# Kernel optimization log

Measured on AMD Instinct MI355X. Metric: run time of the kernel, lower is better.

## Reference

```python
import jax, jax.numpy as jnp
import numpy as np

N_NODES = 20000   # num_of_nodes + 1 (incl. prediction node)
FEAT = 256        # in_features == hidden_features == out_features
N_LAYERS = 2
ALPHA = 0.2       # LeakyReLU negative slope
V_OBS = 512       # observed codes per patient
D_H = np.sqrt(FEAT * 1.0)  # sqrt(hidden_features * num_of_heads), n_heads=1
EPS = 1e-6


def _fc_edges(nodes):
    # torch: source = nodes.repeat(1, n); dest = each node repeated n times
    n = len(nodes)
    return np.stack([np.tile(nodes, n), np.repeat(nodes, n)]).astype(np.int64)


def setup_inputs() -> dict:
    key = jax.random.key(0)
    ks = jax.random.split(key, 16)
    rng = np.random.default_rng(0)
    obs = np.sort(rng.choice(np.arange(1, N_NODES - 1), size=V_OBS, replace=False))
    input_edges = jnp.asarray(_fc_edges(obs))
    obs_out = np.concatenate([obs, [N_NODES - 1]])  # add prediction node
    output_edges = jnp.asarray(_fc_edges(obs_out))

    s = 0.02
    embed = s * jax.random.normal(ks[0], (N_NODES, FEAT), jnp.float32)
    embed = embed.at[0].set(0.0)  # padding_idx=0
    return {
        "embed": embed,
        "W_w": s * jax.random.normal(ks[1], (N_LAYERS, FEAT, FEAT), jnp.float32),
        "W_b": s * jax.random.normal(ks[2], (N_LAYERS, FEAT), jnp.float32),
        "a": s * jax.random.normal(ks[3], (N_LAYERS, 2 * FEAT), jnp.float32),
        "ln_a": jnp.ones((N_LAYERS, FEAT), jnp.float32),
        "ln_b": jnp.zeros((N_LAYERS, FEAT), jnp.float32),
        "Wo_w": s * jax.random.normal(ks[4], (FEAT, FEAT), jnp.float32),
        "Wo_b": s * jax.random.normal(ks[5], (FEAT,), jnp.float32),
        "ao": s * jax.random.normal(ks[6], (2 * FEAT,), jnp.float32),
        "lno_a": jnp.ones((FEAT,), jnp.float32),
        "lno_b": jnp.zeros((FEAT,), jnp.float32),
        "lin_w": s * jax.random.normal(ks[7], (FEAT, FEAT), jnp.float32),
        "lin_b": s * jax.random.normal(ks[8], (FEAT,), jnp.float32),
        "param_w": s * jax.random.normal(ks[9], (2 * FEAT, FEAT), jnp.float32),
        "param_b": s * jax.random.normal(ks[10], (2 * FEAT,), jnp.float32),
        "out1_w": s * jax.random.normal(ks[11], (FEAT, FEAT), jnp.float32),
        "out1_b": s * jax.random.normal(ks[12], (FEAT,), jnp.float32),
        "out2_w": s * jax.random.normal(ks[13], (1, FEAT), jnp.float32),
        "out2_b": s * jax.random.normal(ks[14], (1,), jnp.float32),
        "input_edges": input_edges,
        "output_edges": output_edges,
    }


def _attention(x, edges, Ww, Wb, avec):
    # d = Linear(x): (N, H)
    d = x @ Ww.T + Wb
    H = d.shape[1]
    # a . [d_src ; d_dst] == (d @ a_left)[src] + (d @ a_right)[dst]  (cheaper, same math)
    s_node = d @ avec[:H]
    t_node = d @ avec[H:]
    score = s_node[edges[0]] + t_node[edges[1]]                  # (E,)
    e = jnp.exp(jax.nn.leaky_relu(score, ALPHA) / D_H)           # unnormalized attn
    n = x.shape[0]
    rowsum = jax.ops.segment_sum(e, edges[0], num_segments=n)   # (N,)
    agg = jax.ops.segment_sum(e[:, None] * d[edges[1]], edges[0], num_segments=n)
    zero = rowsum == 0
    # rows with no in-edges get an identity self-edge of weight 1 and rowsum 1
    agg = agg + jnp.where(zero[:, None], d, 0.0)
    return agg / jnp.where(zero, 1.0, rowsum)[:, None]


def _layernorm(x, g, b):
    m = x.mean(-1, keepdims=True)
    s = jnp.std(x, axis=-1, ddof=1, keepdims=True)  # torch std: unbiased
    return g * (x - m) / (s + EPS) + b


def reference(embed, W_w, W_b, a, ln_a, ln_b, Wo_w, Wo_b, ao, lno_a, lno_b,
              lin_w, lin_b, param_w, param_b, out1_w, out1_b, out2_w, out2_b,
              input_edges, output_edges):
    h = embed  # embedding lookup of arange(N) == the full table
    for l in range(N_LAYERS):  # in_att stack, concat=True, n_heads=1: ffn = LN -> ELU
        h = jax.nn.elu(_layernorm(_attention(h, input_edges, W_w[l], W_b[l], a[l]),
                                  ln_a[l], ln_b[l]))
    # variational layer (eval mode: reparameterize returns mu)
    hp = (h @ param_w.T + param_b).reshape(-1, 2, FEAT)
    h = hp[:, 0, :]  # mu
    # out_att: concat=False, mean over 1 head; ffn = LN -> ReLU -> Linear
    g = _attention(h, output_edges, Wo_w, Wo_b, ao)
    g = jax.nn.relu(_layernorm(g, lno_a, lno_b)) @ lin_w.T + lin_b
    # out_layer on prediction node: ReLU -> Linear -> ReLU -> Linear(->1)
    z = jax.nn.relu(g[-1])
    z = jax.nn.relu(z @ out1_w.T + out1_b)
    logit = z @ out2_w.T + out2_b  # (1,)
    return logit
```

## Files before the change

kernel.cpp:

```cpp
#include <hip/hip_runtime.h>
#include <hip/hip_bf16.h>

#define FEAT 256
#define NOBS 512
#define NOUT 513
#define GAT_ALPHA 0.2f
#define INV_DH (1.0f / 16.0f)
#define LN_EPS 1e-6f


__device__ __forceinline__ float b2f(unsigned short u) {
    union { float f; unsigned v; } x;
    x.v = ((unsigned)u) << 16;
    return x.f;
}

__device__ __forceinline__ float loadv(const void* p, long idx, int isbf) {
    if (isbf) return b2f(((const unsigned short*)p)[idx]);
    return ((const float*)p)[idx];
}

__device__ __forceinline__ float4 load4(const void* p, long idx, int isbf) {
    if (isbf) {
        ushort4 u = *(const ushort4*)((const unsigned short*)p + idx);
        return make_float4(b2f(u.x), b2f(u.y), b2f(u.z), b2f(u.w));
    }
    return *(const float4*)((const float*)p + idx);
}

__device__ __forceinline__ int detect_bf(const void* w) {
    const unsigned short* hb = (const unsigned short*)w;
    int sane = 0;
#pragma unroll
    for (int i = 0; i < 32; i += 2) {
        float a = fabsf(b2f(hb[i]));
        sane += (a > 1e-4f && a < 0.3f) ? 1 : 0;
    }
    return (sane >= 8) ? 1 : 0;
}

__device__ __forceinline__ int detect_estep(const void* edges) {
    const int* ei = (const int*)edges;
    return (ei[1] == 0 && ei[3] == 0 && ei[5] == 0 && ei[7] == 0) ? 2 : 1;
}

__device__ __forceinline__ float wave_allreduce(float v) {
#pragma unroll
    for (int o = 1; o < 64; o <<= 1) v += __shfl_xor(v, o);
    return v;
}

__device__ __forceinline__ float bsum1024(float v, float* red) {
    __syncthreads();
    float s = wave_allreduce(v);
    int lane = threadIdx.x & 63, w = threadIdx.x >> 6;
    if (lane == 0) red[w] = s;
    __syncthreads();
    float t = 0.f;
#pragma unroll
    for (int i = 0; i < 16; i++) t += red[i];
    return t;
}

#define FV_AS0 0
#define FV_AS1 256
#define FV_AT0 512
#define FV_AT1 768
#define FV_WB0 1024
#define FV_WB1 1280
#define FV_LNA0 1536
#define FV_LNA1 1792
#define FV_LNB0 2048
#define FV_LNB1 2304
#define FV_WOB 2560
#define FV_AOS 2816
#define FV_AOT 3072
#define FV_LNOA 3328
#define FV_LNOB 3584
#define FV_LINB 3840
#define FV_PARB 4096
#define FV_O1B 4352
#define FV_O2W 4608
#define FV_O2B 4864

__global__ __launch_bounds__(256) void k_front(
        const void* embed, const void* W_w, const void* W_b, const void* a,
        const void* ln_a, const void* ln_b, const void* Wo_w, const void* Wo_b,
        const void* ao, const void* lno_a, const void* lno_b, const void* lin_w,
        const void* lin_b, const void* param_w, const void* param_b,
        const void* out1_w, const void* out1_b, const void* out2_w, const void* out2_b,
        const void* oedges, float* fv, float* packs,
        float* __restrict__ D1, float* S1, float* T1, int* done) {
    __shared__ __align__(16) char smem[37888];
    float (*xs)[FEAT] = (float(*)[FEAT])smem;
    float (*wl)[33] = (float(*)[33])(smem + 4096);
    float (*tile)[65] = (float(*)[65])smem;
    int isbf = detect_bf(W_w);
    int b = blockIdx.x, tid = threadIdx.x, lane = tid & 63, w = tid >> 6;
    if (b < 129) {
        int estep = detect_estep(oedges);
        int i0 = b << 2;
        int nr = NOUT - i0;
        if (nr > 4) nr = 4;
        if (w < nr) {
            const int* oe = (const int*)oedges;
            long node = oe[(long)(i0 + w) * estep];
            *(float4*)&xs[w][lane << 2] = load4(embed, node * FEAT + (lane << 2), isbf);
        } else {
#pragma unroll
            for (int q = 0; q < 4; q++) xs[w][(lane << 2) + q] = 0.f;
        }
        float acc[4] = {0.f, 0.f, 0.f, 0.f};
        int fb8 = tid >> 3;
        int kq = tid & 7;
        for (int kc = 0; kc < 8; kc++) {
            int k0 = kc << 5;
            __syncthreads();
#pragma unroll
            for (int i = 0; i < 8; i++) {
                int f = fb8 + (i << 5);
                float4 v = load4(W_w, (long)f * FEAT + k0 + (kq << 2), isbf);
                wl[f][(kq << 2) + 0] = v.x;
                wl[f][(kq << 2) + 1] = v.y;
                wl[f][(kq << 2) + 2] = v.z;
                wl[f][(kq << 2) + 3] = v.w;
            }
            __syncthreads();
#pragma unroll
            for (int k4 = 0; k4 < 8; k4++) {
                float4 x0 = ((const float4*)xs[0])[(kc << 3) + k4];
                float4 x1 = ((const float4*)xs[1])[(kc << 3) + k4];
                float4 x2 = ((const float4*)xs[2])[(kc << 3) + k4];
                float4 x3 = ((const float4*)xs[3])[(kc << 3) + k4];
                float xa0[4] = {x0.x, x0.y, x0.z, x0.w};
                float xa1[4] = {x1.x, x1.y, x1.z, x1.w};
                float xa2[4] = {x2.x, x2.y, x2.z, x2.w};
                float xa3[4] = {x3.x, x3.y, x3.z, x3.w};
#pragma unroll
                for (int j = 0; j < 4; j++) {
                    float wv = wl[tid][(k4 << 2) + j];
                    acc[0] += xa0[j] * wv;
                    acc[1] += xa1[j] * wv;
                    acc[2] += xa2[j] * wv;
                    acc[3] += xa3[j] * wv;
                }
            }
        }
        float bb = loadv(W_b, tid, isbf);
#pragma unroll
        for (int j = 0; j < 4; j++) acc[j] += bb;
#pragma unroll
        for (int j = 0; j < 4; j++)
            if (j < nr) D1[(long)(i0 + j) * FEAT + tid] = acc[j];
        __syncthreads();
#pragma unroll
        for (int j = 0; j < 4; j++) xs[j][tid] = acc[j];
        __syncthreads();
        if (w < nr) {
            float sv = 0.f, tv = 0.f;
#pragma unroll
            for (int q = 0; q < 4; q++) {
                int f = lane + (q << 6);
                float dv = xs[w][f];
                sv += dv * loadv(a, f, isbf);
                tv += dv * loadv(a, FEAT + f, isbf);
            }
            sv = wave_allreduce(sv);
            tv = wave_allreduce(tv);
            if (lane == 0) { S1[i0 + w] = sv; T1[i0 + w] = tv; }
        }
    } else if (b < 209) {
        int job = b - 129;
        int m = 1 + (job >> 4), t = job & 15;
        int f0 = (t >> 2) << 6, k0 = (t & 3) << 6;
        const void* base;
        long eoff = 0;
        switch (m) {
            case 1: base = W_w; eoff = 65536; break;
            case 2: base = param_w; break;
            case 3: base = Wo_w; break;
            case 4: base = lin_w; break;
            default: base = out1_w; break;
        }
        int r = tid >> 2, cq = (tid & 3) << 4;
#pragma unroll
        for (int jj = 0; jj < 4; jj++) {
            float4 v = load4(base, eoff + (long)(f0 + r) * FEAT + k0 + cq + (jj << 2), isbf);
            tile[r][cq + (jj << 2) + 0] = v.x;
            tile[r][cq + (jj << 2) + 1] = v.y;
            tile[r][cq + (jj << 2) + 2] = v.z;
            tile[r][cq + (jj << 2) + 3] = v.w;
        }
        __syncthreads();
        float4* pack = (float4*)(packs + (long)m * 65536);
#pragma unroll
        for (int it = 0; it < 4; it++) {
            int kk = ((w << 2) + it) << 2;
            float4 v = make_float4(tile[lane][kk], tile[lane][kk + 1],
                                   tile[lane][kk + 2], tile[lane][kk + 3]);
            int k4g = (k0 >> 2) + (w << 2) + it;
            pack[(k4g << 8) + f0 + lane] = v;
        }
    } else {
        int cid = b - 209;
        const void* s;
        long so = 0;
        float* d;
        int n = 256;
        switch (cid) {
            case 0:  s = a;       so = 0;   d = fv + FV_AS0;  break;
            case 1:  s = a;       so = 512; d = fv + FV_AS1;  break;
            case 2:  s = a;       so = 256; d = fv + FV_AT0;  break;
            case 3:  s = a;       so = 768; d = fv + FV_AT1;  break;
            case 4:  s = W_b;     so = 0;   d = fv + FV_WB0;  break;
            case 5:  s = W_b;     so = 256; d = fv + FV_WB1;  break;
            case 6:  s = ln_a;    so = 0;   d = fv + FV_LNA0; break;
            case 7:  s = ln_a;    so = 256; d = fv + FV_LNA1; break;
            case 8:  s = ln_b;    so = 0;   d = fv + FV_LNB0; break;
            case 9:  s = ln_b;    so = 256; d = fv + FV_LNB1; break;
            case 10: s = Wo_b;    so = 0;   d = fv + FV_WOB;  break;
            case 11: s = ao;      so = 0;   d = fv + FV_AOS;  break;
            case 12: s = ao;      so = 256; d = fv + FV_AOT;  break;
            case 13: s = lno_a;   so = 0;   d = fv + FV_LNOA; break;
            case 14: s = lno_b;   so = 0;   d = fv + FV_LNOB; break;
            case 15: s = lin_b;   so = 0;   d = fv + FV_LINB; break;
            case 16: s = param_b; so = 0;   d = fv + FV_PARB; break;
            case 17: s = out1_b;  so = 0;   d = fv + FV_O1B;  break;
            case 18: s = out2_w;  so = 0;   d = fv + FV_O2W;  break;
            default: s = out2_b;  so = 0;   d = fv + FV_O2B;  n = 1; break;
        }
        for (int idx = tid; idx < n; idx += FEAT) d[idx] = loadv(s, so + idx, isbf);
        if (cid == 19 && tid == 0)
            __hip_atomic_store(done, 0, __ATOMIC_RELAXED, __HIP_MEMORY_SCOPE_AGENT);
    }
}

__device__ void tail_head(const float* __restrict__ D, const float* __restrict__ S,
                          const float* __restrict__ T, const float* __restrict__ fv,
                          const float4* __restrict__ PL, const float4* __restrict__ PO1,
                          int isbf, void* out, float* e, float (*wacc)[FEAT],
                          float (*part)[FEAT], float* ys, float* zs, float* red) {
    int tid = threadIdx.x, lane = tid & 63, w = tid >> 6;
    float sN = S[NOUT - 1];
    float p = 0.f;
    if (tid < NOUT) {
        float sc = sN + T[tid];
        sc = (sc > 0.f ? sc : GAT_ALPHA * sc) * INV_DH;
        float ev = __expf(sc);
        e[tid] = ev;
        p = ev;
    }
    float rowsum = bsum1024(p, red);
    float4 a4 = make_float4(0.f, 0.f, 0.f, 0.f);
    for (int j = w; j < NOUT; j += 16) {
        float ej = e[j];
        float4 dv = *(const float4*)(D + (long)j * FEAT + (lane << 2));
        a4.x += ej * dv.x; a4.y += ej * dv.y;
        a4.z += ej * dv.z; a4.w += ej * dv.w;
    }
    *(float4*)&wacc[w][lane << 2] = a4;
    __syncthreads();
    float val = 0.f;
    if (tid < FEAT) {
#pragma unroll
        for (int q = 0; q < 16; q++) val += wacc[q][tid];
        val /= rowsum;
    }
    float m = bsum1024(tid < FEAT ? val : 0.f, red) * (1.f / FEAT);
    float dv = (tid < FEAT) ? val - m : 0.f;
    float var = bsum1024(dv * dv, red) * (1.f / (FEAT - 1));
    if (tid < FEAT) {
        float y = fv[FV_LNOA + tid] * dv / (sqrtf(var) + LN_EPS) + fv[FV_LNOB + tid];
        ys[tid] = fmaxf(y, 0.f);
    }
    __syncthreads();
    int f = tid & 255, kq = tid >> 8;
    float g = 0.f;
#pragma unroll
    for (int q = 0; q < 16; q++) {
        int k4 = (kq << 4) + q;
        float4 wv = PL[(k4 << 8) + f];
        float4 yv = ((const float4*)ys)[k4];
        g += yv.x * wv.x + yv.y * wv.y + yv.z * wv.z + yv.w * wv.w;
    }
    part[kq][f] = g;
    __syncthreads();
    if (tid < FEAT) {
        float gg = part[0][tid] + part[1][tid] + part[2][tid] + part[3][tid] + fv[FV_LINB + tid];
        zs[tid] = fmaxf(gg, 0.f);
    }
    __syncthreads();
    float g2 = 0.f;
#pragma unroll
    for (int q = 0; q < 16; q++) {
        int k4 = (kq << 4) + q;
        float4 wv = PO1[(k4 << 8) + f];
        float4 zv = ((const float4*)zs)[k4];
        g2 += zv.x * wv.x + zv.y * wv.y + zv.z * wv.z + zv.w * wv.w;
    }
    __syncthreads();
    part[kq][f] = g2;
    __syncthreads();
    float z2 = 0.f;
    if (tid < FEAT) {
        z2 = part[0][tid] + part[1][tid] + part[2][tid] + part[3][tid] + fv[FV_O1B + tid];
        z2 = fmaxf(z2, 0.f);
        z2 *= fv[FV_O2W + tid];
    }
    float logit = bsum1024(z2, red) + fv[FV_O2B];
    if (tid == 0) {
        if (isbf) ((__hip_bfloat16*)out)[0] = __float2bfloat16(logit);
        else ((float*)out)[0] = logit;
    }
}

template <bool PWO, bool TAIL>
__global__ __launch_bounds__(1024) void k_mid(
        const float* __restrict__ Din, const float* __restrict__ Sin,
        const float* __restrict__ Tin, const float* __restrict__ ga,
        const float* __restrict__ gb, const float4* __restrict__ W1,
        const float* __restrict__ b1, const float4* __restrict__ W2,
        const float* __restrict__ b2v, const float* __restrict__ as_,
        const float* __restrict__ at_, float* __restrict__ Dout,
        float* Sout, float* Tout,
        const float* fvFull, const float4* PL, const float4* PO1,
        const void* dtypeP, int* done, void* out) {
    __shared__ __align__(16) float e[2][NOBS];
    __shared__ __align__(16) float sacc[16][2][FEAT];
    __shared__ __align__(16) float xs[2][FEAT];
    __shared__ __align__(16) float part[4][2][FEAT];
    __shared__ float redA[16];
    __shared__ float redB[16];
    __shared__ float rsh[2];
    __shared__ int lastflag;
    int tid = threadIdx.x, lane = tid & 63, w = tid >> 6;
    int b = blockIdx.x;
    bool fb = (b == 256);
    int i0 = b << 1;
    int nr = fb ? 1 : 2;
    int row = (tid >> 8) & 1, f = tid & 255;

    float val = 0.f;
    if (!fb) {
        int rr = tid >> 9, j = tid & 511;
        float sc = Sin[i0 + rr] + Tin[j];
        sc = (sc > 0.f ? sc : GAT_ALPHA * sc) * INV_DH;
        e[rr][j] = __expf(sc);
        __syncthreads();
        int r2 = w >> 3, seg = w & 7;
        float pv = wave_allreduce(e[r2][(seg << 6) + lane]);
        if (lane == 0) redA[w] = pv;
        __syncthreads();
        if (tid < 2) {
            float s = 0.f;
#pragma unroll
            for (int q = 0; q < 8; q++) s += redA[(tid << 3) + q];
            rsh[tid] = s;
        }
        float4 a0 = make_float4(0.f, 0.f, 0.f, 0.f), a1 = a0;
        for (int j2 = w; j2 < NOBS; j2 += 16) {
            float4 dv = *(const float4*)(Din + (long)j2 * FEAT + (lane << 2));
            float e0 = e[0][j2], e1 = e[1][j2];
            a0.x += e0 * dv.x; a0.y += e0 * dv.y; a0.z += e0 * dv.z; a0.w += e0 * dv.w;
            a1.x += e1 * dv.x; a1.y += e1 * dv.y; a1.z += e1 * dv.z; a1.w += e1 * dv.w;
        }
        *(float4*)&sacc[w][0][lane << 2] = a0;
        *(float4*)&sacc[w][1][lane << 2] = a1;
        __syncthreads();
        if (tid < 512) {
#pragma unroll
            for (int q = 0; q < 16; q++) val += sacc[q][row][f];
            val /= rsh[row];
        }
    } else {
        if (tid < 512) val = (row == 0) ? Din[(long)NOBS * FEAT + f] : 0.f;
    }

    __syncthreads();
    float s1 = wave_allreduce(tid < 512 ? val : 0.f);
    if (lane == 0) redA[w] = s1;
    __syncthreads();
    float m = (redA[(row << 2)] + redA[(row << 2) + 1] +
               redA[(row << 2) + 2] + redA[(row << 2) + 3]) * (1.f / FEAT);
    float dvv = (tid < 512) ? val - m : 0.f;
    __syncthreads();
    float s2 = wave_allreduce(dvv * dvv);
    if (lane == 0) redA[w] = s2;
    __syncthreads();
    float var = (redA[(row << 2)] + redA[(row << 2) + 1] +
                 redA[(row << 2) + 2] + redA[(row << 2) + 3]) * (1.f / (FEAT - 1));
    if (tid < 512) {
        float isd = 1.f / (sqrtf(var) + LN_EPS);
        float y = ga[f] * dvv * isd + gb[f];
        xs[row][f] = (y > 0.f) ? y : (__expf(y) - 1.f);
    }
    __syncthreads();

    int q = tid >> 8;
    float ac0 = 0.f, ac1 = 0.f;
#pragma unroll
    for (int t = 0; t < 16; t++) {
        int k4 = (q << 4) + t;
        float4 wv = W1[(k4 << 8) + f];
        float4 x0 = ((const float4*)xs[0])[k4];
        float4 x1 = ((const float4*)xs[1])[k4];
        ac0 += x0.x * wv.x + x0.y * wv.y + x0.z * wv.z + x0.w * wv.w;
        ac1 += x1.x * wv.x + x1.y * wv.y + x1.z * wv.z + x1.w * wv.w;
    }
    part[q][0][f] = ac0;
    part[q][1][f] = ac1;
    __syncthreads();
    float dval = 0.f;
    if (tid < 512)
        dval = part[0][row][f] + part[1][row][f] + part[2][row][f] + part[3][row][f] + b1[f];
    if (PWO) {
        __syncthreads();
        if (tid < 512) xs[row][f] = dval;
        __syncthreads();
        float bc0 = 0.f, bc1 = 0.f;
#pragma unroll
        for (int t = 0; t < 16; t++) {
            int k4 = (q << 4) + t;
            float4 wv = W2[(k4 << 8) + f];
            float4 x0 = ((const float4*)xs[0])[k4];
            float4 x1 = ((const float4*)xs[1])[k4];
            bc0 += x0.x * wv.x + x0.y * wv.y + x0.z * wv.z + x0.w * wv.w;
            bc1 += x1.x * wv.x + x1.y * wv.y + x1.z * wv.z + x1.w * wv.w;
        }
        __syncthreads();
        part[q][0][f] = bc0;
        part[q][1][f] = bc1;
        __syncthreads();
        if (tid < 512)
            dval = part[0][row][f] + part[1][row][f] + part[2][row][f] + part[3][row][f] + b2v[f];
    }
    if (tid < 512 && row < nr)
        Dout[(long)(i0 + row) * FEAT + f] = dval;

    __syncthreads();
    float sv = wave_allreduce(tid < 512 ? dval * as_[f] : 0.f);
    float tv = wave_allreduce(tid < 512 ? dval * at_[f] : 0.f);
    if (lane == 0) { redA[w] = sv; redB[w] = tv; }
    __syncthreads();
    if (tid < nr) {
        float ss = redA[(tid << 2)] + redA[(tid << 2) + 1] +
                   redA[(tid << 2) + 2] + redA[(tid << 2) + 3];
        float tt = redB[(tid << 2)] + redB[(tid << 2) + 1] +
                   redB[(tid << 2) + 2] + redB[(tid << 2) + 3];
        Sout[i0 + tid] = ss;
        Tout[i0 + tid] = tt;
    }

    if (TAIL) {
        __syncthreads();
        if (tid == 0) {
            __threadfence();
            int old = atomicAdd(done, 1);
            lastflag = (old == 256) ? 1 : 0;
        }
        __syncthreads();
        if (lastflag) {
            if (tid == 0) __threadfence();
            __syncthreads();
            int isbf = detect_bf(dtypeP);
            tail_head(Dout, Sout, Tout, fvFull, PL, PO1, isbf, out,
                      (float*)e, (float(*)[FEAT])sacc, (float(*)[FEAT])part,
                      (float*)part + 4 * FEAT, (float*)part + 5 * FEAT, redA);
        }
    }
}

extern "C" void kernel_launch(void* const* d_in, const int* in_sizes, int n_in,
                              void* d_out, int out_size, void* d_ws, size_t ws_size,
                              hipStream_t stream) {
    const void* embed = d_in[0];
    const void* W_w = d_in[1];
    const void* W_b = d_in[2];
    const void* a = d_in[3];
    const void* ln_a = d_in[4];
    const void* ln_b = d_in[5];
    const void* Wo_w = d_in[6];
    const void* Wo_b = d_in[7];
    const void* ao = d_in[8];
    const void* lno_a = d_in[9];
    const void* lno_b = d_in[10];
    const void* lin_w = d_in[11];
    const void* lin_b = d_in[12];
    const void* param_w = d_in[13];
    const void* param_b = d_in[14];
    const void* out1_w = d_in[15];
    const void* out1_b = d_in[16];
    const void* out2_w = d_in[17];
    const void* out2_b = d_in[18];
    const void* oedges = d_in[20];

    char* ws = (char*)d_ws;
    int* done = (int*)ws;
    float* fv = (float*)(ws + 256);
    float* packs = (float*)(ws + 32768);
    float* D1 = (float*)(ws + 1605632);
    float* D2 = (float*)(ws + 2131200);
    float* S1 = (float*)(ws + 2656768);
    float* T1 = (float*)(ws + 2660864);
    float* S2 = (float*)(ws + 2664960);
    float* T2 = (float*)(ws + 2669056);

    const float4* P1 = (const float4*)(packs + 1 * 65536);
    const float4* PP = (const float4*)(packs + 2 * 65536);
    const float4* PWo = (const float4*)(packs + 3 * 65536);
    const float4* PL = (const float4*)(packs + 4 * 65536);
    const float4* PO1 = (const float4*)(packs + 5 * 65536);

    k_front<<<229, FEAT, 0, stream>>>(embed, W_w, W_b, a, ln_a, ln_b, Wo_w, Wo_b, ao,
                                      lno_a, lno_b, lin_w, lin_b, param_w, param_b,
                                      out1_w, out1_b, out2_w, out2_b, oedges,
                                      fv, packs, D1, S1, T1, done);
    k_mid<false, false><<<257, 1024, 0, stream>>>(D1, S1, T1, fv + FV_LNA0, fv + FV_LNB0,
                                                  P1, fv + FV_WB1, nullptr, nullptr,
                                                  fv + FV_AS1, fv + FV_AT1, D2, S2, T2,
                                                  nullptr, nullptr, nullptr, nullptr,
                                                  nullptr, nullptr);
    k_mid<true, true><<<257, 1024, 0, stream>>>(D2, S2, T2, fv + FV_LNA1, fv + FV_LNB1,
                                                PP, fv + FV_PARB, PWo, fv + FV_WOB,
                                                fv + FV_AOS, fv + FV_AOT, D1, S1, T1,
                                                fv, PL, PO1, W_w, done, d_out);
}
```

Baseline: 96.88 us.

## Fuse three kernels into one persistent kernel with software grid barriers

Replaces the front kernel and the two mid kernels with a single 256-block persistent kernel. The stages are separated by atomic-counter grid barriers, and a memset resets the counters before launch. The prediction node's row is now computed by the last-finishing block through a serial chain of matrix-vector products instead of as an extra block in each stage, and stores use nontemporal hints. This aims to remove kernel launch gaps and the odd 257th block, at the cost of spin-wait barriers that depend on all 256 blocks being co-resident and on a serial tail.

```diff
diff --git a/kernel.cpp b/kernel.cpp
--- a/kernel.cpp
+++ b/kernel.cpp
@@ -4,9 +4,12 @@
 #define FEAT 256
 #define NOBS 512
 #define NOUT 513
+#define NBLK 256
 #define GAT_ALPHA 0.2f
 #define INV_DH (1.0f / 16.0f)
 #define LN_EPS 1e-6f
+
+typedef float f32x4 __attribute__((ext_vector_type(4)));
 
 
 __device__ __forceinline__ float b2f(unsigned short u) {
@@ -60,6 +63,24 @@
 #pragma unroll
     for (int i = 0; i < 16; i++) t += red[i];
     return t;
+}
+
+__device__ __forceinline__ void ntst(float* p, float v) { __builtin_nontemporal_store(v, p); }
+__device__ __forceinline__ void ntst4(float* p, float4 v) {
+    f32x4 t = {v.x, v.y, v.z, v.w};
+    __builtin_nontemporal_store(t, (f32x4*)p);
+}
+
+__device__ __forceinline__ void gsync(int* bar, int idx) {
+    __syncthreads();
+    if (threadIdx.x == 0) {
+        __threadfence();
+        atomicAdd(&bar[idx], 1);
+        while (__hip_atomic_load(&bar[idx], __ATOMIC_RELAXED, __HIP_MEMORY_SCOPE_AGENT) < NBLK)
+            __builtin_amdgcn_s_sleep(2);
+        __threadfence();
+    }
+    __syncthreads();
 }
 
 #define FV_AS0 0
@@ -83,126 +104,297 @@
 #define FV_O2W 4608
 #define FV_O2B 4864
 
-__global__ __launch_bounds__(256) void k_front(
+#define O_E 0
+#define O_SACC 4096
+#define O_XS 36864
+#define O_PART 38912
+#define O_REDA 47104
+#define O_REDB 47168
+#define O_RSH 47232
+#define O_FLAG 47240
+#define SMEM_BYTES 47360
+
+__device__ __forceinline__ void mv1024(const float4* __restrict__ P, const float* __restrict__ bias,
+                                       const float* __restrict__ xin, float* __restrict__ dst,
+                                       float (*part)[FEAT]) {
+    int tid = threadIdx.x, f = tid & 255, kq = tid >> 8;
+    float g = 0.f;
+#pragma unroll
+    for (int t = 0; t < 16; t++) {
+        int k4 = (kq << 4) + t;
+        float4 wv = P[(k4 << 8) + f];
+        float4 xv = ((const float4*)xin)[k4];
+        g += xv.x * wv.x + xv.y * wv.y + xv.z * wv.z + xv.w * wv.w;
+    }
+    __syncthreads();
+    part[kq][f] = g;
+    __syncthreads();
+    if (tid < FEAT) dst[tid] = part[0][tid] + part[1][tid] + part[2][tid] + part[3][tid] + bias[tid];
+    __syncthreads();
+}
+
+__device__ __forceinline__ void ln_elu(float* v, const float* ga, const float* gb, float* red) {
+    int tid = threadIdx.x;
+    float x = (tid < FEAT) ? v[tid] : 0.f;
+    float m = bsum1024(x, red) * (1.f / FEAT);
+    float d = (tid < FEAT) ? x - m : 0.f;
+    float var = bsum1024(d * d, red) * (1.f / (FEAT - 1));
+    if (tid < FEAT) {
+        float y = ga[tid] * d / (sqrtf(var) + LN_EPS) + gb[tid];
+        v[tid] = (y > 0.f) ? y : (__expf(y) - 1.f);
+    }
+    __syncthreads();
+}
+
+template <bool PWO>
+__device__ __forceinline__ void stage_mid(char* smem,
+        const float* __restrict__ Din, const float* __restrict__ Sin,
+        const float* __restrict__ Tin, const float* __restrict__ ga,
+        const float* __restrict__ gb, const float4* __restrict__ W1,
+        const float* __restrict__ b1, const float4* __restrict__ W2,
+        const float* __restrict__ b2v, const float* __restrict__ as_,
+        const float* __restrict__ at_, float* __restrict__ Dout,
+        float* Sout, float* Tout) {
+    float (*e)[NOBS] = (float(*)[NOBS])(smem + O_E);
+    float (*sacc)[2][FEAT] = (float(*)[2][FEAT])(smem + O_SACC);
+    float (*xs)[FEAT] = (float(*)[FEAT])(smem + O_XS);
+    float (*part)[2][FEAT] = (float(*)[2][FEAT])(smem + O_PART);
+    float* redA = (float*)(smem + O_REDA);
+    float* redB = (float*)(smem + O_REDB);
+    float* rsh = (float*)(smem + O_RSH);
+    int tid = threadIdx.x, lane = tid & 63, w = tid >> 6;
+    int b = blockIdx.x;
+    int i0 = b << 1;
+    int row = (tid >> 8) & 1, f = tid & 255;
+
+    int rr = tid >> 9, j = tid & 511;
+    float sc = Sin[i0 + rr] + Tin[j];
+    sc = (sc > 0.f ? sc : GAT_ALPHA * sc) * INV_DH;
+    e[rr][j] = __expf(sc);
+    __syncthreads();
+    int r2 = w >> 3, seg = w & 7;
+    float pv = wave_allreduce(e[r2][(seg << 6) + lane]);
+    if (lane == 0) redA[w] = pv;
+    __syncthreads();
+    if (tid < 2) {
+        float s = 0.f;
+#pragma unroll
+        for (int q = 0; q < 8; q++) s += redA[(tid << 3) + q];
+        rsh[tid] = s;
+    }
+    float4 a0 = make_float4(0.f, 0.f, 0.f, 0.f), a1 = a0;
+    for (int j2 = w; j2 < NOBS; j2 += 16) {
+        float4 dv = *(const float4*)(Din + (long)j2 * FEAT + (lane << 2));
+        float e0 = e[0][j2], e1 = e[1][j2];
+        a0.x += e0 * dv.x; a0.y += e0 * dv.y; a0.z += e0 * dv.z; a0.w += e0 * dv.w;
+        a1.x += e1 * dv.x; a1.y += e1 * dv.y; a1.z += e1 * dv.z; a1.w += e1 * dv.w;
+    }
+    *(float4*)&sacc[w][0][lane << 2] = a0;
+    *(float4*)&sacc[w][1][lane << 2] = a1;
+    __syncthreads();
+    float val = 0.f;
+    if (tid < 512) {
+#pragma unroll
+        for (int q = 0; q < 16; q++) val += sacc[q][row][f];
+        val /= rsh[row];
+    }
+    __syncthreads();
+    float s1 = wave_allreduce(tid < 512 ? val : 0.f);
+    if (lane == 0) redA[w] = s1;
+    __syncthreads();
+    float m = (redA[(row << 2)] + redA[(row << 2) + 1] +
+               redA[(row << 2) + 2] + redA[(row << 2) + 3]) * (1.f / FEAT);
+    float dvv = (tid < 512) ? val - m : 0.f;
+    __syncthreads();
+    float s2 = wave_allreduce(dvv * dvv);
+    if (lane == 0) redA[w] = s2;
+    __syncthreads();
+    float var = (redA[(row << 2)] + redA[(row << 2) + 1] +
+                 redA[(row << 2) + 2] + redA[(row << 2) + 3]) * (1.f / (FEAT - 1));
+    if (tid < 512) {
+        float isd = 1.f / (sqrtf(var) + LN_EPS);
+        float y = ga[f] * dvv * isd + gb[f];
+        xs[row][f] = (y > 0.f) ? y : (__expf(y) - 1.f);
+    }
+    __syncthreads();
+    int q = tid >> 8;
+    float ac0 = 0.f, ac1 = 0.f;
+#pragma unroll
+    for (int t = 0; t < 16; t++) {
+        int k4 = (q << 4) + t;
+        float4 wv = W1[(k4 << 8) + f];
+        float4 x0 = ((const float4*)xs[0])[k4];
+        float4 x1 = ((const float4*)xs[1])[k4];
+        ac0 += x0.x * wv.x + x0.y * wv.y + x0.z * wv.z + x0.w * wv.w;
+        ac1 += x1.x * wv.x + x1.y * wv.y + x1.z * wv.z + x1.w * wv.w;
+    }
+    part[q][0][f] = ac0;
+    part[q][1][f] = ac1;
+    __syncthreads();
+    float dval = 0.f;
+    if (tid < 512)
+        dval = part[0][row][f] + part[1][row][f] + part[2][row][f] + part[3][row][f] + b1[f];
+    if (PWO) {
+        __syncthreads();
+        if (tid < 512) xs[row][f] = dval;
+        __syncthreads();
+        float bc0 = 0.f, bc1 = 0.f;
+#pragma unroll
+        for (int t = 0; t < 16; t++) {
+            int k4 = (q << 4) + t;
+            float4 wv = W2[(k4 << 8) + f];
+            float4 x0 = ((const float4*)xs[0])[k4];
+            float4 x1 = ((const float4*)xs[1])[k4];
+            bc0 += x0.x * wv.x + x0.y * wv.y + x0.z * wv.z + x0.w * wv.w;
+            bc1 += x1.x * wv.x + x1.y * wv.y + x1.z * wv.z + x1.w * wv.w;
+        }
+        __syncthreads();
+        part[q][0][f] = bc0;
+        part[q][1][f] = bc1;
+        __syncthreads();
+        if (tid < 512)
+            dval = part[0][row][f] + part[1][row][f] + part[2][row][f] + part[3][row][f] + b2v[f];
+    }
+    if (tid < 512) ntst(&Dout[(long)(i0 + row) * FEAT + f], dval);
+    __syncthreads();
+    float sv = wave_allreduce(tid < 512 ? dval * as_[f] : 0.f);
+    float tv = wave_allreduce(tid < 512 ? dval * at_[f] : 0.f);
+    if (lane == 0) { redA[w] = sv; redB[w] = tv; }
+    __syncthreads();
+    if (tid < 2) {
+        float ss = redA[(tid << 2)] + redA[(tid << 2) + 1] +
+                   redA[(tid << 2) + 2] + redA[(tid << 2) + 3];
+        float tt = redB[(tid << 2)] + redB[(tid << 2) + 1] +
+                   redB[(tid << 2) + 2] + redB[(tid << 2) + 3];
+        ntst(&Sout[i0 + tid], ss);
+        ntst(&Tout[i0 + tid], tt);
+    }
+}
+
+__device__ void tail_head(const float* __restrict__ D, const float* __restrict__ S,
+                          const float* __restrict__ T, const float* __restrict__ fv,
+                          const float4* __restrict__ PL, const float4* __restrict__ PO1,
+                          int isbf, void* out, float* e, float (*wacc)[FEAT],
+                          float (*part)[FEAT], float* ys, float* zs, float* red) {
+    int tid = threadIdx.x, lane = tid & 63, w = tid >> 6;
+    float sN = S[NOUT - 1];
+    float p = 0.f;
+    if (tid < NOUT) {
+        float sc = sN + T[tid];
+        sc = (sc > 0.f ? sc : GAT_ALPHA * sc) * INV_DH;
+        float ev = __expf(sc);
+        e[tid] = ev;
+        p = ev;
+    }
+    float rowsum = bsum1024(p, red);
+    float4 a4 = make_float4(0.f, 0.f, 0.f, 0.f);
+    for (int j = w; j < NOUT; j += 16) {
+        float ej = e[j];
+        float4 dv = *(const float4*)(D + (long)j * FEAT + (lane << 2));
+        a4.x += ej * dv.x; a4.y += ej * dv.y;
+        a4.z += ej * dv.z; a4.w += ej * dv.w;
+    }
+    *(float4*)&wacc[w][lane << 2] = a4;
+    __syncthreads();
+    float val = 0.f;
+    if (tid < FEAT) {
+#pragma unroll
+        for (int q = 0; q < 16; q++) val += wacc[q][tid];
+        val /= rowsum;
+    }
+    float m = bsum1024(tid < FEAT ? val : 0.f, red) * (1.f / FEAT);
+    float dv = (tid < FEAT) ? val - m : 0.f;
+    float var = bsum1024(dv * dv, red) * (1.f / (FEAT - 1));
+    if (tid < FEAT) {
+        float y = fv[FV_LNOA + tid] * dv / (sqrtf(var) + LN_EPS) + fv[FV_LNOB + tid];
+        ys[tid] = fmaxf(y, 0.f);
+    }
+    __syncthreads();
+    int f = tid & 255, kq = tid >> 8;
+    float g = 0.f;
+#pragma unroll
+    for (int q = 0; q < 16; q++) {
+        int k4 = (kq << 4) + q;
+        float4 wv = PL[(k4 << 8) + f];
+        float4 yv = ((const float4*)ys)[k4];
+        g += yv.x * wv.x + yv.y * wv.y + yv.z * wv.z + yv.w * wv.w;
+    }
+    part[kq][f] = g;
+    __syncthreads();
+    if (tid < FEAT) {
+        float gg = part[0][tid] + part[1][tid] + part[2][tid] + part[3][tid] + fv[FV_LINB + tid];
+        zs[tid] = fmaxf(gg, 0.f);
+    }
+    __syncthreads();
+    float g2 = 0.f;
+#pragma unroll
+    for (int q = 0; q < 16; q++) {
+        int k4 = (kq << 4) + q;
+        float4 wv = PO1[(k4 << 8) + f];
+        float4 zv = ((const float4*)zs)[k4];
+        g2 += zv.x * wv.x + zv.y * wv.y + zv.z * wv.z + zv.w * wv.w;
+    }
+    __syncthreads();
+    part[kq][f] = g2;
+    __syncthreads();
+    float z2 = 0.f;
+    if (tid < FEAT) {
+        z2 = part[0][tid] + part[1][tid] + part[2][tid] + part[3][tid] + fv[FV_O1B + tid];
+        z2 = fmaxf(z2, 0.f);
+        z2 *= fv[FV_O2W + tid];
+    }
+    float logit = bsum1024(z2, red) + fv[FV_O2B];
+    if (tid == 0) {
+        if (isbf) ((__hip_bfloat16*)out)[0] = __float2bfloat16(logit);
+        else ((float*)out)[0] = logit;
+    }
+}
+
+__global__ __launch_bounds__(1024) void k_all(
         const void* embed, const void* W_w, const void* W_b, const void* a,
         const void* ln_a, const void* ln_b, const void* Wo_w, const void* Wo_b,
         const void* ao, const void* lno_a, const void* lno_b, const void* lin_w,
         const void* lin_b, const void* param_w, const void* param_b,
         const void* out1_w, const void* out1_b, const void* out2_w, const void* out2_b,
-        const void* oedges, float* fv, float* packs,
-        float* __restrict__ D1, float* S1, float* T1, int* done) {
-    __shared__ __align__(16) char smem[37888];
-    float (*xs)[FEAT] = (float(*)[FEAT])smem;
-    float (*wl)[33] = (float(*)[33])(smem + 4096);
-    float (*tile)[65] = (float(*)[65])smem;
+        const void* oedges, int* bar, float* fv, float* packs,
+        float* D1, float* S1, float* T1, float* D2, float* S2, float* T2,
+        float* D3, float* S3, float* T3, void* out) {
+    __shared__ __align__(16) char smem[SMEM_BYTES];
+    int tid = threadIdx.x, lane = tid & 63, w = tid >> 6, b = blockIdx.x;
     int isbf = detect_bf(W_w);
-    int b = blockIdx.x, tid = threadIdx.x, lane = tid & 63, w = tid >> 6;
-    if (b < 129) {
-        int estep = detect_estep(oedges);
-        int i0 = b << 2;
-        int nr = NOUT - i0;
-        if (nr > 4) nr = 4;
-        if (w < nr) {
-            const int* oe = (const int*)oedges;
-            long node = oe[(long)(i0 + w) * estep];
-            *(float4*)&xs[w][lane << 2] = load4(embed, node * FEAT + (lane << 2), isbf);
-        } else {
-#pragma unroll
-            for (int q = 0; q < 4; q++) xs[w][(lane << 2) + q] = 0.f;
-        }
-        float acc[4] = {0.f, 0.f, 0.f, 0.f};
-        int fb8 = tid >> 3;
-        int kq = tid & 7;
-        for (int kc = 0; kc < 8; kc++) {
-            int k0 = kc << 5;
-            __syncthreads();
-#pragma unroll
-            for (int i = 0; i < 8; i++) {
-                int f = fb8 + (i << 5);
-                float4 v = load4(W_w, (long)f * FEAT + k0 + (kq << 2), isbf);
-                wl[f][(kq << 2) + 0] = v.x;
-                wl[f][(kq << 2) + 1] = v.y;
-                wl[f][(kq << 2) + 2] = v.z;
-                wl[f][(kq << 2) + 3] = v.w;
-            }
-            __syncthreads();
-#pragma unroll
-            for (int k4 = 0; k4 < 8; k4++) {
-                float4 x0 = ((const float4*)xs[0])[(kc << 3) + k4];
-                float4 x1 = ((const float4*)xs[1])[(kc << 3) + k4];
-                float4 x2 = ((const float4*)xs[2])[(kc << 3) + k4];
-                float4 x3 = ((const float4*)xs[3])[(kc << 3) + k4];
-                float xa0[4] = {x0.x, x0.y, x0.z, x0.w};
-                float xa1[4] = {x1.x, x1.y, x1.z, x1.w};
-                float xa2[4] = {x2.x, x2.y, x2.z, x2.w};
-                float xa3[4] = {x3.x, x3.y, x3.z, x3.w};
-#pragma unroll
-                for (int j = 0; j < 4; j++) {
-                    float wv = wl[tid][(k4 << 2) + j];
-                    acc[0] += xa0[j] * wv;
-                    acc[1] += xa1[j] * wv;
-                    acc[2] += xa2[j] * wv;
-                    acc[3] += xa3[j] * wv;
-                }
-            }
-        }
-        float bb = loadv(W_b, tid, isbf);
-#pragma unroll
-        for (int j = 0; j < 4; j++) acc[j] += bb;
-#pragma unroll
-        for (int j = 0; j < 4; j++)
-            if (j < nr) D1[(long)(i0 + j) * FEAT + tid] = acc[j];
-        __syncthreads();
-#pragma unroll
-        for (int j = 0; j < 4; j++) xs[j][tid] = acc[j];
-        __syncthreads();
-        if (w < nr) {
-            float sv = 0.f, tv = 0.f;
-#pragma unroll
-            for (int q = 0; q < 4; q++) {
-                int f = lane + (q << 6);
-                float dv = xs[w][f];
-                sv += dv * loadv(a, f, isbf);
-                tv += dv * loadv(a, FEAT + f, isbf);
-            }
-            sv = wave_allreduce(sv);
-            tv = wave_allreduce(tv);
-            if (lane == 0) { S1[i0 + w] = sv; T1[i0 + w] = tv; }
-        }
-    } else if (b < 209) {
-        int job = b - 129;
-        int m = 1 + (job >> 4), t = job & 15;
+    const float4* P0 = (const float4*)(packs);
+    const float4* P1 = (const float4*)(packs + 65536);
+    const float4* PP = (const float4*)(packs + 2 * 65536);
+    const float4* PWo = (const float4*)(packs + 3 * 65536);
+    const float4* PL = (const float4*)(packs + 4 * 65536);
+    const float4* PO1 = (const float4*)(packs + 5 * 65536);
+
+    if (b < 96) {
+        float (*tile)[65] = (float(*)[65])smem;
+        int m = b >> 4, t = b & 15;
         int f0 = (t >> 2) << 6, k0 = (t & 3) << 6;
         const void* base;
         long eoff = 0;
         switch (m) {
+            case 0: base = W_w; break;
             case 1: base = W_w; eoff = 65536; break;
             case 2: base = param_w; break;
             case 3: base = Wo_w; break;
             case 4: base = lin_w; break;
             default: base = out1_w; break;
         }
-        int r = tid >> 2, cq = (tid & 3) << 4;
-#pragma unroll
-        for (int jj = 0; jj < 4; jj++) {
-            float4 v = load4(base, eoff + (long)(f0 + r) * FEAT + k0 + cq + (jj << 2), isbf);
-            tile[r][cq + (jj << 2) + 0] = v.x;
-            tile[r][cq + (jj << 2) + 1] = v.y;
-            tile[r][cq + (jj << 2) + 2] = v.z;
-            tile[r][cq + (jj << 2) + 3] = v.w;
-        }
-        __syncthreads();
-        float4* pack = (float4*)(packs + (long)m * 65536);
-#pragma unroll
-        for (int it = 0; it < 4; it++) {
-            int kk = ((w << 2) + it) << 2;
-            float4 v = make_float4(tile[lane][kk], tile[lane][kk + 1],
-                                   tile[lane][kk + 2], tile[lane][kk + 3]);
-            int k4g = (k0 >> 2) + (w << 2) + it;
-            pack[(k4g << 8) + f0 + lane] = v;
-        }
-    } else {
-        int cid = b - 209;
+        int r = tid >> 4, c4 = (tid & 15) << 2;
+        float4 v = load4(base, eoff + (long)(f0 + r) * FEAT + k0 + c4, isbf);
+        tile[r][c4 + 0] = v.x; tile[r][c4 + 1] = v.y;
+        tile[r][c4 + 2] = v.z; tile[r][c4 + 3] = v.w;
+        __syncthreads();
+        int k4l = tid >> 6, fl = tid & 63;
+        int kk = k4l << 2;
+        float4 o = make_float4(tile[fl][kk], tile[fl][kk + 1], tile[fl][kk + 2], tile[fl][kk + 3]);
+        int k4g = (k0 >> 2) + k4l;
+        ntst4(&packs[(long)m * 65536 + (((long)(k4g << 8) + f0 + fl) << 2)], o);
+    } else if (b < 116) {
+        int cid = b - 96;
         const void* s;
         long so = 0;
         float* d;
@@ -229,244 +421,99 @@
             case 18: s = out2_w;  so = 0;   d = fv + FV_O2W;  break;
             default: s = out2_b;  so = 0;   d = fv + FV_O2B;  n = 1; break;
         }
-        for (int idx = tid; idx < n; idx += FEAT) d[idx] = loadv(s, so + idx, isbf);
-        if (cid == 19 && tid == 0)
-            __hip_atomic_store(done, 0, __ATOMIC_RELAXED, __HIP_MEMORY_SCOPE_AGENT);
-    }
-}
-
-__device__ void tail_head(const float* __restrict__ D, const float* __restrict__ S,
-                          const float* __restrict__ T, const float* __restrict__ fv,
-                          const float4* __restrict__ PL, const float4* __restrict__ PO1,
-                          int isbf, void* out, float* e, float (*wacc)[FEAT],
-                          float (*part)[FEAT], float* ys, float* zs, float* red) {
-    int tid = threadIdx.x, lane = tid & 63, w = tid >> 6;
-    float sN = S[NOUT - 1];
-    float p = 0.f;
-    if (tid < NOUT) {
-        float sc = sN + T[tid];
-        sc = (sc > 0.f ? sc : GAT_ALPHA * sc) * INV_DH;
-        float ev = __expf(sc);
-        e[tid] = ev;
-        p = ev;
-    }
-    float rowsum = bsum1024(p, red);
-    float4 a4 = make_float4(0.f, 0.f, 0.f, 0.f);
-    for (int j = w; j < NOUT; j += 16) {
-        float ej = e[j];
-        float4 dv = *(const float4*)(D + (long)j * FEAT + (lane << 2));
-        a4.x += ej * dv.x; a4.y += ej * dv.y;
-        a4.z += ej * dv.z; a4.w += ej * dv.w;
-    }
-    *(float4*)&wacc[w][lane << 2] = a4;
-    __syncthreads();
-    float val = 0.f;
-    if (tid < FEAT) {
-#pragma unroll
-        for (int q = 0; q < 16; q++) val += wacc[q][tid];
-        val /= rowsum;
-    }
-    float m = bsum1024(tid < FEAT ? val : 0.f, red) * (1.f / FEAT);
-    float dv = (tid < FEAT) ? val - m : 0.f;
-    float var = bsum1024(dv * dv, red) * (1.f / (FEAT - 1));
-    if (tid < FEAT) {
-        float y = fv[FV_LNOA + tid] * dv / (sqrtf(var) + LN_EPS) + fv[FV_LNOB + tid];
-        ys[tid] = fmaxf(y, 0.f);
-    }
-    __syncthreads();
-    int f = tid & 255, kq = tid >> 8;
-    float g = 0.f;
-#pragma unroll
-    for (int q = 0; q < 16; q++) {
-        int k4 = (kq << 4) + q;
-        float4 wv = PL[(k4 << 8) + f];
-        float4 yv = ((const float4*)ys)[k4];
-        g += yv.x * wv.x + yv.y * wv.y + yv.z * wv.z + yv.w * wv.w;
-    }
-    part[kq][f] = g;
-    __syncthreads();
-    if (tid < FEAT) {
-        float gg = part[0][tid] + part[1][tid] + part[2][tid] + part[3][tid] + fv[FV_LINB + tid];
-        zs[tid] = fmaxf(gg, 0.f);
-    }
-    __syncthreads();
-    float g2 = 0.f;
-#pragma unroll
-    for (int q = 0; q < 16; q++) {
-        int k4 = (kq << 4) + q;
-        float4 wv = PO1[(k4 << 8) + f];
-        float4 zv = ((const float4*)zs)[k4];
-        g2 += zv.x * wv.x + zv.y * wv.y + zv.z * wv.z + zv.w * wv.w;
-    }
-    __syncthreads();
-    part[kq][f] = g2;
-    __syncthreads();
-    float z2 = 0.f;
-    if (tid < FEAT) {
-        z2 = part[0][tid] + part[1][tid] + part[2][tid] + part[3][tid] + fv[FV_O1B + tid];
-        z2 = fmaxf(z2, 0.f);
-        z2 *= fv[FV_O2W + tid];
-    }
-    float logit = bsum1024(z2, red) + fv[FV_O2B];
+        for (int idx = tid; idx < n; idx += 1024) ntst(&d[idx], loadv(s, so + idx, isbf));
+    }
+    gsync(bar, 0);
+
+    if (b < 128) {
+        int estep = detect_estep(oedges);
+        float (*xs)[FEAT] = (float(*)[FEAT])smem;
+        float (*part)[4][FEAT] = (float(*)[4][FEAT])(smem + 4096);
+        float* redA = (float*)(smem + O_REDA);
+        float* redB = (float*)(smem + O_REDB);
+        int i0 = b << 2;
+        int row = tid >> 8, f = tid & 255;
+        const int* oe = (const int*)oedges;
+        long node = oe[(long)(i0 + row) * estep];
+        xs[row][f] = loadv(embed, node * FEAT + f, isbf);
+        __syncthreads();
+        int kq = tid >> 8;
+        float ac[4] = {0.f, 0.f, 0.f, 0.f};
+#pragma unroll
+        for (int t = 0; t < 16; t++) {
+            int k4 = (kq << 4) + t;
+            float4 wv = P0[(k4 << 8) + f];
+#pragma unroll
+            for (int r = 0; r < 4; r++) {
+                float4 xv = ((const float4*)xs[r])[k4];
+                ac[r] += xv.x * wv.x + xv.y * wv.y + xv.z * wv.z + xv.w * wv.w;
+            }
+        }
+#pragma unroll
+        for (int r = 0; r < 4; r++) part[kq][r][f] = ac[r];
+        __syncthreads();
+        float dval = part[0][row][f] + part[1][row][f] + part[2][row][f] + part[3][row][f]
+                     + fv[FV_WB0 + f];
+        ntst(&D1[(long)(i0 + row) * FEAT + f], dval);
+        float sv = wave_allreduce(dval * fv[FV_AS0 + f]);
+        float tv = wave_allreduce(dval * fv[FV_AT0 + f]);
+        if (lane == 0) { redA[w] = sv; redB[w] = tv; }
+        __syncthreads();
+        if (tid < 4) {
+            float ss = redA[(tid << 2)] + redA[(tid << 2) + 1] +
+                       redA[(tid << 2) + 2] + redA[(tid << 2) + 3];
+            float tt = redB[(tid << 2)] + redB[(tid << 2) + 1] +
+                       redB[(tid << 2) + 2] + redB[(tid << 2) + 3];
+            ntst(&S1[i0 + tid], ss);
+            ntst(&T1[i0 + tid], tt);
+        }
+    }
+    gsync(bar, 1);
+
+    stage_mid<false>(smem, D1, S1, T1, fv + FV_LNA0, fv + FV_LNB0, P1, fv + FV_WB1,
+                     nullptr, nullptr, fv + FV_AS1, fv + FV_AT1, D2, S2, T2);
+    gsync(bar, 2);
+    stage_mid<true>(smem, D2, S2, T2, fv + FV_LNA1, fv + FV_LNB1, PP, fv + FV_PARB,
+                    PWo, fv + FV_WOB, fv + FV_AOS, fv + FV_AOT, D3, S3, T3);
+
+    __syncthreads();
+    int* lastflag = (int*)(smem + O_FLAG);
     if (tid == 0) {
-        if (isbf) ((__hip_bfloat16*)out)[0] = __float2bfloat16(logit);
-        else ((float*)out)[0] = logit;
-    }
-}
-
-template <bool PWO, bool TAIL>
-__global__ __launch_bounds__(1024) void k_mid(
-        const float* __restrict__ Din, const float* __restrict__ Sin,
-        const float* __restrict__ Tin, const float* __restrict__ ga,
-        const float* __restrict__ gb, const float4* __restrict__ W1,
-        const float* __restrict__ b1, const float4* __restrict__ W2,
-        const float* __restrict__ b2v, const float* __restrict__ as_,
-        const float* __restrict__ at_, float* __restrict__ Dout,
-        float* Sout, float* Tout,
-        const float* fvFull, const float4* PL, const float4* PO1,
-        const void* dtypeP, int* done, void* out) {
-    __shared__ __align__(16) float e[2][NOBS];
-    __shared__ __align__(16) float sacc[16][2][FEAT];
-    __shared__ __align__(16) float xs[2][FEAT];
-    __shared__ __align__(16) float part[4][2][FEAT];
-    __shared__ float redA[16];
-    __shared__ float redB[16];
-    __shared__ float rsh[2];
-    __shared__ int lastflag;
-    int tid = threadIdx.x, lane = tid & 63, w = tid >> 6;
-    int b = blockIdx.x;
-    bool fb = (b == 256);
-    int i0 = b << 1;
-    int nr = fb ? 1 : 2;
-    int row = (tid >> 8) & 1, f = tid & 255;
-
-    float val = 0.f;
-    if (!fb) {
-        int rr = tid >> 9, j = tid & 511;
-        float sc = Sin[i0 + rr] + Tin[j];
-        sc = (sc > 0.f ? sc : GAT_ALPHA * sc) * INV_DH;
-        e[rr][j] = __expf(sc);
-        __syncthreads();
-        int r2 = w >> 3, seg = w & 7;
-        float pv = wave_allreduce(e[r2][(seg << 6) + lane]);
-        if (lane == 0) redA[w] = pv;
-        __syncthreads();
-        if (tid < 2) {
-            float s = 0.f;
-#pragma unroll
-            for (int q = 0; q < 8; q++) s += redA[(tid << 3) + q];
-            rsh[tid] = s;
-        }
-        float4 a0 = make_float4(0.f, 0.f, 0.f, 0.f), a1 = a0;
-        for (int j2 = w; j2 < NOBS; j2 += 16) {
-            float4 dv = *(const float4*)(Din + (long)j2 * FEAT + (lane << 2));
-            float e0 = e[0][j2], e1 = e[1][j2];
-            a0.x += e0 * dv.x; a0.y += e0 * dv.y; a0.z += e0 * dv.z; a0.w += e0 * dv.w;
-            a1.x += e1 * dv.x; a1.y += e1 * dv.y; a1.z += e1 * dv.z; a1.w += e1 * dv.w;
-        }
-        *(float4*)&sacc[w][0][lane << 2] = a0;
-        *(float4*)&sacc[w][1][lane << 2] = a1;
-        __syncthreads();
-        if (tid < 512) {
-#pragma unroll
-            for (int q = 0; q < 16; q++) val += sacc[q][row][f];
-            val /= rsh[row];
-        }
-    } else {
-        if (tid < 512) val = (row == 0) ? Din[(long)NOBS * FEAT + f] : 0.f;
-    }
-
-    __syncthreads();
-    float s1 = wave_allreduce(tid < 512 ? val : 0.f);
-    if (lane == 0) redA[w] = s1;
-    __syncthreads();
-    float m = (redA[(row << 2)] + redA[(row << 2) + 1] +
-               redA[(row << 2) + 2] + redA[(row << 2) + 3]) * (1.f / FEAT);
-    float dvv = (tid < 512) ? val - m : 0.f;
-    __syncthreads();
-    float s2 = wave_allreduce(dvv * dvv);
-    if (lane == 0) redA[w] = s2;
-    __syncthreads();
-    float var = (redA[(row << 2)] + redA[(row << 2) + 1] +
-                 redA[(row << 2) + 2] + redA[(row << 2) + 3]) * (1.f / (FEAT - 1));
-    if (tid < 512) {
-        float isd = 1.f / (sqrtf(var) + LN_EPS);
-        float y = ga[f] * dvv * isd + gb[f];
-        xs[row][f] = (y > 0.f) ? y : (__expf(y) - 1.f);
-    }
-    __syncthreads();
-
-    int q = tid >> 8;
-    float ac0 = 0.f, ac1 = 0.f;
-#pragma unroll
-    for (int t = 0; t < 16; t++) {
-        int k4 = (q << 4) + t;
-        float4 wv = W1[(k4 << 8) + f];
-        float4 x0 = ((const float4*)xs[0])[k4];
-        float4 x1 = ((const float4*)xs[1])[k4];
-        ac0 += x0.x * wv.x + x0.y * wv.y + x0.z * wv.z + x0.w * wv.w;
-        ac1 += x1.x * wv.x + x1.y * wv.y + x1.z * wv.z + x1.w * wv.w;
-    }
-    part[q][0][f] = ac0;
-    part[q][1][f] = ac1;
-    __syncthreads();
-    float dval = 0.f;
-    if (tid < 512)
-        dval = part[0][row][f] + part[1][row][f] + part[2][row][f] + part[3][row][f] + b1[f];
-    if (PWO) {
-        __syncthreads();
-        if (tid < 512) xs[row][f] = dval;
-        __syncthreads();
-        float bc0 = 0.f, bc1 = 0.f;
-#pragma unroll
-        for (int t = 0; t < 16; t++) {
-            int k4 = (q << 4) + t;
-            float4 wv = W2[(k4 << 8) + f];
-            float4 x0 = ((const float4*)xs[0])[k4];
-            float4 x1 = ((const float4*)xs[1])[k4];
-            bc0 += x0.x * wv.x + x0.y * wv.y + x0.z * wv.z + x0.w * wv.w;
-            bc1 += x1.x * wv.x + x1.y * wv.y + x1.z * wv.z + x1.w * wv.w;
-        }
-        __syncthreads();
-        part[q][0][f] = bc0;
-        part[q][1][f] = bc1;
-        __syncthreads();
-        if (tid < 512)
-            dval = part[0][row][f] + part[1][row][f] + part[2][row][f] + part[3][row][f] + b2v[f];
-    }
-    if (tid < 512 && row < nr)
-        Dout[(long)(i0 + row) * FEAT + f] = dval;
-
-    __syncthreads();
-    float sv = wave_allreduce(tid < 512 ? dval * as_[f] : 0.f);
-    float tv = wave_allreduce(tid < 512 ? dval * at_[f] : 0.f);
-    if (lane == 0) { redA[w] = sv; redB[w] = tv; }
-    __syncthreads();
-    if (tid < nr) {
-        float ss = redA[(tid << 2)] + redA[(tid << 2) + 1] +
-                   redA[(tid << 2) + 2] + redA[(tid << 2) + 3];
-        float tt = redB[(tid << 2)] + redB[(tid << 2) + 1] +
-                   redB[(tid << 2) + 2] + redB[(tid << 2) + 3];
-        Sout[i0 + tid] = ss;
-        Tout[i0 + tid] = tt;
-    }
-
-    if (TAIL) {
-        __syncthreads();
-        if (tid == 0) {
-            __threadfence();
-            int old = atomicAdd(done, 1);
-            lastflag = (old == 256) ? 1 : 0;
-        }
-        __syncthreads();
-        if (lastflag) {
-            if (tid == 0) __threadfence();
-            __syncthreads();
-            int isbf = detect_bf(dtypeP);
-            tail_head(Dout, Sout, Tout, fvFull, PL, PO1, isbf, out,
-                      (float*)e, (float(*)[FEAT])sacc, (float(*)[FEAT])part,
-                      (float*)part + 4 * FEAT, (float*)part + 5 * FEAT, redA);
-        }
+        __threadfence();
+        int old = atomicAdd(&bar[3], 1);
+        *lastflag = (old == NBLK - 1) ? 1 : 0;
+    }
+    __syncthreads();
+    if (*lastflag) {
+        if (tid == 0) __threadfence();
+        __syncthreads();
+        float* ys = (float*)(smem + O_XS);
+        float* zs = (float*)(smem + O_XS + 1024);
+        float (*mvp)[FEAT] = (float(*)[FEAT])(smem + O_PART);
+        float* red = (float*)(smem + O_REDA);
+        int estep = detect_estep(oedges);
+        const int* oe = (const int*)oedges;
+        long node = oe[(long)(NOUT - 1) * estep];
+        if (tid < FEAT) ys[tid] = loadv(embed, node * FEAT + tid, isbf);
+        __syncthreads();
+        mv1024(P0, fv + FV_WB0, ys, zs, mvp);
+        ln_elu(zs, fv + FV_LNA0, fv + FV_LNB0, red);
+        mv1024(P1, fv + FV_WB1, zs, ys, mvp);
+        ln_elu(ys, fv + FV_LNA1, fv + FV_LNB1, red);
+        mv1024(PP, fv + FV_PARB, ys, zs, mvp);
+        mv1024(PWo, fv + FV_WOB, zs, ys, mvp);
+        float sv = bsum1024(tid < FEAT ? ys[tid] * fv[FV_AOS + tid] : 0.f, red);
+        float tv = bsum1024(tid < FEAT ? ys[tid] * fv[FV_AOT + tid] : 0.f, red);
+        if (tid < FEAT) D3[(long)NOBS * FEAT + tid] = ys[tid];
+        if (tid == 0) { S3[NOUT - 1] = sv; T3[NOUT - 1] = tv; }
+        __syncthreads();
+        tail_head(D3, S3, T3, fv, PL, PO1, isbf, out,
+                  (float*)(smem + O_E),
+                  (float(*)[FEAT])(smem + O_SACC),
+                  (float(*)[FEAT])(smem + O_PART),
+                  (float*)(smem + O_PART + 4096),
+                  (float*)(smem + O_PART + 5120),
+                  (float*)(smem + O_REDA));
     }
 }
 
@@ -495,33 +542,23 @@
     const void* oedges = d_in[20];
 
     char* ws = (char*)d_ws;
-    int* done = (int*)ws;
+    int* bar = (int*)ws;
     float* fv = (float*)(ws + 256);
     float* packs = (float*)(ws + 32768);
     float* D1 = (float*)(ws + 1605632);
-    float* D2 = (float*)(ws + 2131200);
-    float* S1 = (float*)(ws + 2656768);
-    float* T1 = (float*)(ws + 2660864);
-    float* S2 = (float*)(ws + 2664960);
-    float* T2 = (float*)(ws + 2669056);
-
-    const float4* P1 = (const float4*)(packs + 1 * 65536);
-    const float4* PP = (const float4*)(packs + 2 * 65536);
-    const float4* PWo = (const float4*)(packs + 3 * 65536);
-    const float4* PL = (const float4*)(packs + 4 * 65536);
-    const float4* PO1 = (const float4*)(packs + 5 * 65536);
-
-    k_front<<<229, FEAT, 0, stream>>>(embed, W_w, W_b, a, ln_a, ln_b, Wo_w, Wo_b, ao,
-                                      lno_a, lno_b, lin_w, lin_b, param_w, param_b,
-                                      out1_w, out1_b, out2_w, out2_b, oedges,
-                                      fv, packs, D1, S1, T1, done);
-    k_mid<false, false><<<257, 1024, 0, stream>>>(D1, S1, T1, fv + FV_LNA0, fv + FV_LNB0,
-                                                  P1, fv + FV_WB1, nullptr, nullptr,
-                                                  fv + FV_AS1, fv + FV_AT1, D2, S2, T2,
-                                                  nullptr, nullptr, nullptr, nullptr,
-                                                  nullptr, nullptr);
-    k_mid<true, true><<<257, 1024, 0, stream>>>(D2, S2, T2, fv + FV_LNA1, fv + FV_LNB1,
-                                                PP, fv + FV_PARB, PWo, fv + FV_WOB,
-                                                fv + FV_AOS, fv + FV_AOT, D1, S1, T1,
-                                                fv, PL, PO1, W_w, done, d_out);
-}
+    float* D2 = (float*)(ws + 2134016);
+    float* D3 = (float*)(ws + 2662400);
+    float* S1 = (float*)(ws + 3190784);
+    float* T1 = (float*)(ws + 3193344);
+    float* S2 = (float*)(ws + 3195904);
+    float* T2 = (float*)(ws + 3198464);
+    float* S3 = (float*)(ws + 3201024);
+    float* T3 = (float*)(ws + 3203584);
+
+    hipMemsetAsync(bar, 0, 16, stream);
+    k_all<<<NBLK, 1024, 0, stream>>>(embed, W_w, W_b, a, ln_a, ln_b, Wo_w, Wo_b, ao,
+                                     lno_a, lno_b, lin_w, lin_b, param_w, param_b,
+                                     out1_w, out1_b, out2_w, out2_b, oedges,
+                                     bar, fv, packs, D1, S1, T1, D2, S2, T2,
+                                     D3, S3, T3, d_out);
+}
```

After: 186.4 us. 92.4% more time.
